# Optimization experiments

Measured on AMD Instinct MI355X. Metric: run time of the kernel, lower is better.

Reference implementation:

```python
import jax, jax.numpy as jnp
import numpy as np

B, C, O, H, W = 8, 64, 64, 128, 128


def conv3x3(x, w, b):
    # x: [B,Cin,H,W], w: [Cout,Cin,3,3], stride 1, padding 1
    y = jax.lax.conv_general_dilated(
        x, w, window_strides=(1, 1), padding=((1, 1), (1, 1)),
        dimension_numbers=("NCHW", "OIHW", "NCHW"))
    return y + b[None, :, None, None]


def setup_inputs() -> dict:
    key = jax.random.key(0)
    ks = jax.random.split(key, 6)
    fan = C * 9
    x = jax.random.normal(ks[0], (B, C, H, W), dtype=jnp.float32)
    w_main = jax.random.normal(ks[1], (O, C, 3, 3), dtype=jnp.float32) / np.sqrt(fan)
    # small offset weights keep sampled locations near the regular grid (realistic post-training regime)
    w_offset = jax.random.normal(ks[2], (18, C, 3, 3), dtype=jnp.float32) * 0.05 / np.sqrt(fan)
    b_offset = jnp.zeros((18,), dtype=jnp.float32)
    w_mask = jax.random.normal(ks[3], (9, C, 3, 3), dtype=jnp.float32) / np.sqrt(fan)
    b_mask = jnp.zeros((9,), dtype=jnp.float32)
    return {"x": x, "w_main": w_main, "w_offset": w_offset,
            "b_offset": b_offset, "w_mask": w_mask, "b_mask": b_mask}


def deform_conv2d(x, w_main, offset, mask):
    # torchvision.ops.deform_conv2d: kernel 3x3, stride 1, pad 1, dilation 1, no bias
    Bb, Cc, Hh, Ww = x.shape
    Oo = w_main.shape[0]
    off = offset.reshape(Bb, 9, 2, Hh, Ww)
    dy, dx = off[:, :, 0], off[:, :, 1]            # [B,9,H,W]; pairs ordered (y,x), k row-major
    k = jnp.arange(9)
    kh = (k // 3 - 1).astype(x.dtype)              # kernel row offset in {-1,0,1}
    kw = (k % 3 - 1).astype(x.dtype)
    iy = jnp.arange(Hh, dtype=x.dtype)
    ix = jnp.arange(Ww, dtype=x.dtype)
    # sampling positions p = p0 + p_k + delta_p
    py = dy + iy[None, None, :, None] + kh[None, :, None, None]
    px = dx + ix[None, None, None, :] + kw[None, :, None, None]

    y0 = jnp.floor(py)
    x0 = jnp.floor(px)
    ly = py - y0
    lx = px - x0
    y0i = y0.astype(jnp.int32)
    x0i = x0.astype(jnp.int32)
    y1i = y0i + 1
    x1i = x0i + 1

    bidx = jnp.arange(Bb)[:, None, None, None]

    def corner(yi, xi, wgt):
        # zero-padding semantics: out-of-bounds neighbors contribute 0
        valid = (yi >= 0) & (yi < Hh) & (xi >= 0) & (xi < Ww)
        v = x[bidx, :, jnp.clip(yi, 0, Hh - 1), jnp.clip(xi, 0, Ww - 1)]  # [B,9,H,W,C]
        return v * (wgt * valid)[..., None]

    samp = (corner(y0i, x0i, (1 - ly) * (1 - lx))
            + corner(y0i, x1i, (1 - ly) * lx)
            + corner(y1i, x0i, ly * (1 - lx))
            + corner(y1i, x1i, ly * lx))
    samp = samp * mask[..., None]                  # modulation mask (dcn v2)
    # contract sampled patches with weights: [B,9,H,W,C] x [O,C,9] -> [B,O,H,W]
    return jnp.einsum("bkhwc,ock->bohw", samp, w_main.reshape(Oo, Cc, 9))


def reference(x, w_main, w_offset, b_offset, w_mask, b_mask):
    offset = conv3x3(x, w_offset, b_offset)                 # [B,18,H,W]
    mask = jax.nn.sigmoid(conv3x3(x, w_mask, b_mask))       # [B,9,H,W]
    return deform_conv2d(x, w_main, offset, mask)
```

## Files before the change

kernel.cpp:

```cpp
#include <hip/hip_runtime.h>
#include <math.h>

#define BB 8
#define CC 64
#define OO 64
#define HH 128
#define WW 128
#define HW (HH*WW)
#define NPIX (BB*HW)

typedef __bf16 bf16x8 __attribute__((ext_vector_type(8)));
typedef float floatx4 __attribute__((ext_vector_type(4)));
typedef float f32x2 __attribute__((ext_vector_type(2)));
typedef unsigned short ushort_t;

#define XT_BYTES  16777216
#define OM_BYTES  14680064
#define WT_BYTES  73728

__device__ __forceinline__ unsigned short f2b(float f) {
    unsigned u = __float_as_uint(f);
    u += 0x7fffu + ((u >> 16) & 1u);
    return (unsigned short)(u >> 16);
}

__device__ __forceinline__ unsigned cvt_pk_bf16(float lo, float hi) {
    unsigned r;
    asm("v_cvt_pk_bf16_f32 %0, %1, %2" : "=v"(r) : "v"(lo), "v"(hi));
    return r;
}

__device__ __forceinline__ f32x2 pk_fma(f32x2 a, f32x2 b, f32x2 c) {
    f32x2 d;
    asm("v_pk_fma_f32 %0, %1, %2, %3" : "=v"(d) : "v"(a), "v"(b), "v"(c));
    return d;
}

__device__ __forceinline__ f32x2 pk_mul(f32x2 a, f32x2 b) {
    f32x2 d;
    asm("v_pk_mul_f32 %0, %1, %2" : "=v"(d) : "v"(a), "v"(b));
    return d;
}

__global__ __launch_bounds__(256) void prep_kernel(
    const float* __restrict__ x,
    const float* __restrict__ wm, const float* __restrict__ woff,
    const float* __restrict__ wmask,
    ushort_t* __restrict__ xt, ushort_t* __restrict__ wt,
    ushort_t* __restrict__ wb)
{
    __shared__ float tile[64][33];
    int bid = blockIdx.x;
    int t   = threadIdx.x;

    if (bid < 4096) {
        int bh = bid >> 2;
        int w0 = (bid & 3) * 32;
        int b  = bh >> 7;
        int h  = bh & 127;

        {
            int c  = t >> 2;
            int wq = t & 3;
            const float* src = x + (((size_t)(b*CC + c))*HH + h)*WW + (w0 + wq*8);
            float4 v0 = ((const float4*)src)[0];
            float4 v1 = ((const float4*)src)[1];
            int wbse = wq*8;
            tile[c][wbse+0] = v0.x; tile[c][wbse+1] = v0.y;
            tile[c][wbse+2] = v0.z; tile[c][wbse+3] = v0.w;
            tile[c][wbse+4] = v1.x; tile[c][wbse+5] = v1.y;
            tile[c][wbse+6] = v1.z; tile[c][wbse+7] = v1.w;
        }
        __syncthreads();
        {
            int w   = t & 31;
            int cg8 = t >> 5;
            unsigned uu[4];
            #pragma unroll
            for (int j = 0; j < 4; ++j)
                uu[j] = cvt_pk_bf16(tile[cg8*8 + 2*j][w], tile[cg8*8 + 2*j + 1][w]);
            *(uint4*)(xt + (((size_t)(b*HH + h))*WW + (w0 + w))*CC + cg8*8)
                = make_uint4(uu[0], uu[1], uu[2], uu[3]);
        }
    } else {
        int i = (bid - 4096) * 256 + t;
        if (i < 36864) {
            int o = i / 576, k = i % 576, tap = k >> 6, c = k & 63;
            wt[i] = f2b(wm[o*576 + c*9 + tap]);
        }
        int j = i - 36864;
        if (j >= 0 && j < 18432) {
            int o = j / 576, k = j % 576, tap = k >> 6, c = k & 63;
            float v = 0.f;
            if (o < 18)      v = woff[o*576 + c*9 + tap];
            else if (o < 27) v = wmask[(o-18)*576 + c*9 + tap];
            wb[j] = f2b(v);
        }
    }
}

__global__ __launch_bounds__(256) void conv27_kernel(
    const ushort_t* __restrict__ xt, const ushort_t* __restrict__ wb,
    const float* __restrict__ boff, const float* __restrict__ bmsk,
    float* __restrict__ om)
{
    __shared__ ushort_t win[18*18*72];
    int bid = blockIdx.x;
    int b  = bid >> 6;
    int th = (bid >> 3) & 7;
    int tw = bid & 7;
    int h0 = th * 16, w0 = tw * 16;
    int t = threadIdx.x;

    for (int idx = t; idx < 18*18*8; idx += 256) {
        int r   = idx / 144;
        int rem = idx - r*144;
        int col = rem >> 3;
        int ch  = (rem & 7) << 3;
        int y = h0 + r - 1, x = w0 + col - 1;
        uint4 val = make_uint4(0,0,0,0);
        if ((unsigned)y < (unsigned)HH && (unsigned)x < (unsigned)WW)
            val = *(const uint4*)(xt + ((((size_t)b*HH + y)*WW + x) << 6) + ch);
        *(uint4*)(win + (r*18 + col)*72 + ch) = val;
    }
    __syncthreads();

    int lane = t & 63, wv = t >> 6;
    int n = lane & 15, quad = lane >> 4;
    const ushort_t* wb0 = wb + n*576;
    const ushort_t* wb1 = wb + (16 + n)*576;

    floatx4 acc0[4], acc1[4];
    #pragma unroll
    for (int mt = 0; mt < 4; ++mt) {
        acc0[mt] = (floatx4){0.f,0.f,0.f,0.f};
        acc1[mt] = (floatx4){0.f,0.f,0.f,0.f};
    }

    #pragma unroll
    for (int s = 0; s < 18; ++s) {
        int tap  = s >> 1;
        int tr   = tap / 3, tc = tap % 3;
        int coff = (s & 1)*32 + quad*8;
        int kk = tap*64 + coff;
        bf16x8 b0 = *(const bf16x8*)(wb0 + kk);
        bf16x8 b1 = *(const bf16x8*)(wb1 + kk);
        #pragma unroll
        for (int mt = 0; mt < 4; ++mt) {
            int ty = wv*4 + mt;
            bf16x8 a = *(const bf16x8*)(win + ((ty + tr)*18 + (n + tc))*72 + coff);
            acc0[mt] = __builtin_amdgcn_mfma_f32_16x16x32_bf16(a, b0, acc0[mt], 0, 0, 0);
            acc1[mt] = __builtin_amdgcn_mfma_f32_16x16x32_bf16(a, b1, acc1[mt], 0, 0, 0);
        }
    }

    #pragma unroll
    for (int mt = 0; mt < 4; ++mt) {
        int ty = wv*4 + mt;
        #pragma unroll
        for (int r = 0; r < 4; ++r) {
            int tx = quad*4 + r;
            size_t p = ((size_t)(b*HH + h0 + ty))*WW + (w0 + tx);
            float* dst = om + p*28;
            dst[n] = acc0[mt][r] + boff[n];
            int o1 = 16 + n;
            if (o1 < 18) {
                dst[o1] = acc1[mt][r] + boff[o1];
            } else if (o1 < 27) {
                float z = acc1[mt][r] + bmsk[o1 - 18];
                dst[o1] = 1.f / (1.f + expf(-z));
            } else if (o1 == 27) {
                dst[27] = 0.f;
            }
        }
    }
}

#define SROW 200

__global__ __launch_bounds__(256, 3) void deform_kernel(
    const ushort_t* __restrict__ xt, const float* __restrict__ om,
    const ushort_t* __restrict__ wt, float* __restrict__ out)
{
    __shared__ ushort_t samp[64*SROW];

    int t = threadIdx.x;
    int lane = t & 63, wv = t >> 6;
    int bid = blockIdx.x;
    int b  = bid >> 8;
    int th = (bid >> 4) & 15;
    int tw = bid & 15;
    int h0 = th * 8, w0 = tw * 8;

    int pa = t >> 2, cg = t & 3;
    int ph = pa >> 3, pw = pa & 7;
    int h_a = h0 + ph, w_a = w0 + pw;
    const float* omp = om + (((size_t)(b*HH + h_a))*WW + w_a) * 28;
    const ushort_t* xbase = xt + ((size_t)b << 20);

    int n = lane & 15, quad = lane >> 4;
    floatx4 acc[4];
    #pragma unroll
    for (int i = 0; i < 4; ++i) acc[i] = (floatx4){0.f,0.f,0.f,0.f};
    const ushort_t* wrow = wt + (wv*16 + n)*576 + quad*8;

    uint4 q[24];
    float cwv[12];

    auto issue_phase = [&](int pp, const float* dy3, const float* dx3,
                           const float* m3) {
        #pragma unroll
        for (int kk = 0; kk < 3; ++kk) {
            float py = (float)(h_a + pp - 1) + dy3[kk];
            float px = (float)(w_a + kk - 1) + dx3[kk];
            float y0f = floorf(py), x0f = floorf(px);
            float ly = py - y0f, lx = px - x0f;
            int y0 = (int)y0f, x0 = (int)x0f, y1 = y0 + 1, x1 = x0 + 1;
            float vy0 = ((unsigned)y0 < (unsigned)HH) ? 1.f : 0.f;
            float vy1 = ((unsigned)y1 < (unsigned)HH) ? 1.f : 0.f;
            float vx0 = ((unsigned)x0 < (unsigned)WW) ? 1.f : 0.f;
            float vx1 = ((unsigned)x1 < (unsigned)WW) ? 1.f : 0.f;
            float m   = m3[kk];
            cwv[kk*4+0] = (1.f-ly)*(1.f-lx)*vy0*vx0*m;
            cwv[kk*4+1] = (1.f-ly)*lx      *vy0*vx1*m;
            cwv[kk*4+2] = ly*(1.f-lx)      *vy1*vx0*m;
            cwv[kk*4+3] = ly*lx            *vy1*vx1*m;
            int ys[4] = { y0, y0, y1, y1 };
            int xs[4] = { x0, x1, x0, x1 };
            #pragma unroll
            for (int cn = 0; cn < 4; ++cn) {
                int yc = min(max(ys[cn], 0), HH-1);
                int xc = min(max(xs[cn], 0), WW-1);
                const uint4* cp = (const uint4*)(xbase + (((yc << 7) + xc) << 6) + cg*16);
                q[kk*8+2*cn]   = cp[0];
                q[kk*8+2*cn+1] = cp[1];
            }
        }
    };

    float dyv[3], dxv[3], mv[3];
    #pragma unroll
    for (int j = 0; j < 3; ++j) {
        dyv[j] = omp[2*j]; dxv[j] = omp[2*j+1]; mv[j] = omp[18+j];
    }
    issue_phase(0, dyv, dxv, mv);

    #pragma unroll
    for (int p = 0; p < 3; ++p) {
        bf16x8 wf[6];
        #pragma unroll
        for (int s = 0; s < 6; ++s)
            wf[s] = *(const bf16x8*)(wrow + (p*6 + s)*32);

        float dyn_[3], dxn_[3], mn_[3];
        if (p < 2) {
            #pragma unroll
            for (int j = 0; j < 3; ++j) {
                int k2 = 3*(p+1) + j;
                dyn_[j] = omp[2*k2]; dxn_[j] = omp[2*k2+1]; mn_[j] = omp[18+k2];
            }
        }

        if (p) __syncthreads();

        #pragma unroll
        for (int kk = 0; kk < 3; ++kk) {
            f32x2 v2[8];
            {
                f32x2 w2; w2.x = cwv[kk*4+0]; w2.y = cwv[kk*4+0];
                unsigned u0[8] = { q[kk*8+0].x, q[kk*8+0].y, q[kk*8+0].z, q[kk*8+0].w,
                                   q[kk*8+1].x, q[kk*8+1].y, q[kk*8+1].z, q[kk*8+1].w };
                #pragma unroll
                for (int j = 0; j < 8; ++j) {
                    f32x2 f;
                    f.x = __uint_as_float(u0[j] << 16);
                    f.y = __uint_as_float(u0[j] & 0xffff0000u);
                    v2[j] = pk_mul(f, w2);
                }
            }
            #pragma unroll
            for (int cn = 1; cn < 4; ++cn) {
                f32x2 w2; w2.x = cwv[kk*4+cn]; w2.y = cwv[kk*4+cn];
                unsigned u0[8] = { q[kk*8+2*cn].x,   q[kk*8+2*cn].y,
                                   q[kk*8+2*cn].z,   q[kk*8+2*cn].w,
                                   q[kk*8+2*cn+1].x, q[kk*8+2*cn+1].y,
                                   q[kk*8+2*cn+1].z, q[kk*8+2*cn+1].w };
                #pragma unroll
                for (int j = 0; j < 8; ++j) {
                    f32x2 f;
                    f.x = __uint_as_float(u0[j] << 16);
                    f.y = __uint_as_float(u0[j] & 0xffff0000u);
                    v2[j] = pk_fma(f, w2, v2[j]);
                }
            }
            unsigned uu[8];
            #pragma unroll
            for (int j = 0; j < 8; ++j)
                uu[j] = cvt_pk_bf16(v2[j].x, v2[j].y);
            uint4* dst = (uint4*)(samp + pa*SROW + kk*64 + cg*16);
            dst[0] = make_uint4(uu[0], uu[1], uu[2], uu[3]);
            dst[1] = make_uint4(uu[4], uu[5], uu[6], uu[7]);
        }

        if (p < 2) issue_phase(p+1, dyn_, dxn_, mn_);

        __syncthreads();

        __builtin_amdgcn_s_setprio(1);
        #pragma unroll
        for (int kk = 0; kk < 3; ++kk) {
            #pragma unroll
            for (int half = 0; half < 2; ++half) {
                bf16x8 bfrag = wf[kk*2 + half];
                #pragma unroll
                for (int mt = 0; mt < 4; ++mt) {
                    bf16x8 afrag = *(const bf16x8*)(samp + (mt*16 + n)*SROW
                                                    + kk*64 + half*32 + quad*8);
                    acc[mt] = __builtin_amdgcn_mfma_f32_16x16x32_bf16(
                                  afrag, bfrag, acc[mt], 0, 0, 0);
                }
            }
        }
        __builtin_amdgcn_s_setprio(0);
    }

    float* op = out + ((size_t)b*OO + (wv*16 + n))*HW;
    #pragma unroll
    for (int mt = 0; mt < 4; ++mt) {
        int row = h0 + mt*2 + (quad >> 1);
        int col = w0 + (quad & 1)*4;
        float4 st = make_float4(acc[mt][0], acc[mt][1], acc[mt][2], acc[mt][3]);
        *(float4*)(op + row*WW + col) = st;
    }
}

extern "C" void kernel_launch(void* const* d_in, const int* in_sizes, int n_in,
                              void* d_out, int out_size, void* d_ws, size_t ws_size,
                              hipStream_t stream)
{
    const float* x      = (const float*)d_in[0];
    const float* w_main = (const float*)d_in[1];
    const float* w_off  = (const float*)d_in[2];
    const float* b_off  = (const float*)d_in[3];
    const float* w_msk  = (const float*)d_in[4];
    const float* b_msk  = (const float*)d_in[5];
    float* out = (float*)d_out;

    unsigned char* ws = (unsigned char*)d_ws;
    ushort_t* xt = (ushort_t*)ws;
    float*    om = (float*)(ws + XT_BYTES);
    ushort_t* wt = (ushort_t*)(ws + XT_BYTES + OM_BYTES);
    ushort_t* wb = (ushort_t*)(ws + XT_BYTES + OM_BYTES + WT_BYTES);

    prep_kernel<<<4096 + 216, 256, 0, stream>>>(x, w_main, w_off, w_msk, xt, wt, wb);

    conv27_kernel<<<NPIX/256, 256, 0, stream>>>(xt, wb, b_off, b_msk, om);

    deform_kernel<<<NPIX/64, 256, 0, stream>>>(xt, om, wt, out);
}
```

Before: 175.8 us.

## Pipeline bilinear gathers per tap with double-buffered registers instead of per-row phases

```diff
diff --git a/kernel.cpp b/kernel.cpp
--- a/kernel.cpp
+++ b/kernel.cpp
@@ -176,6 +176,74 @@
     }
 }
 
+__device__ __forceinline__ void issue_tap(
+    uint4* q, float* cw,
+    const ushort_t* xbase, int cg, int h_a, int w_a,
+    int kr, int kc, float dy, float dx, float m)
+{
+    float py = (float)(h_a + kr - 1) + dy;
+    float px = (float)(w_a + kc - 1) + dx;
+    float y0f = floorf(py), x0f = floorf(px);
+    float ly = py - y0f, lx = px - x0f;
+    int y0 = (int)y0f, x0 = (int)x0f, y1 = y0 + 1, x1 = x0 + 1;
+    float vy0 = ((unsigned)y0 < (unsigned)HH) ? 1.f : 0.f;
+    float vy1 = ((unsigned)y1 < (unsigned)HH) ? 1.f : 0.f;
+    float vx0 = ((unsigned)x0 < (unsigned)WW) ? 1.f : 0.f;
+    float vx1 = ((unsigned)x1 < (unsigned)WW) ? 1.f : 0.f;
+    cw[0] = (1.f-ly)*(1.f-lx)*vy0*vx0*m;
+    cw[1] = (1.f-ly)*lx      *vy0*vx1*m;
+    cw[2] = ly*(1.f-lx)      *vy1*vx0*m;
+    cw[3] = ly*lx            *vy1*vx1*m;
+    int ys[4] = { y0, y0, y1, y1 };
+    int xs[4] = { x0, x1, x0, x1 };
+    #pragma unroll
+    for (int cn = 0; cn < 4; ++cn) {
+        int yc = min(max(ys[cn], 0), HH-1);
+        int xc = min(max(xs[cn], 0), WW-1);
+        const uint4* cp = (const uint4*)(xbase + (((yc << 7) + xc) << 6) + cg*16);
+        q[2*cn]   = cp[0];
+        q[2*cn+1] = cp[1];
+    }
+}
+
+__device__ __forceinline__ void pack_tap(
+    const uint4* q, const float* cw, ushort_t* dst)
+{
+    f32x2 v2[8];
+    {
+        f32x2 w2; w2.x = cw[0]; w2.y = cw[0];
+        unsigned u0[8] = { q[0].x, q[0].y, q[0].z, q[0].w,
+                           q[1].x, q[1].y, q[1].z, q[1].w };
+        #pragma unroll
+        for (int j = 0; j < 8; ++j) {
+            f32x2 f;
+            f.x = __uint_as_float(u0[j] << 16);
+            f.y = __uint_as_float(u0[j] & 0xffff0000u);
+            v2[j] = pk_mul(f, w2);
+        }
+    }
+    #pragma unroll
+    for (int cn = 1; cn < 4; ++cn) {
+        f32x2 w2; w2.x = cw[cn]; w2.y = cw[cn];
+        unsigned u0[8] = { q[2*cn].x,   q[2*cn].y,   q[2*cn].z,   q[2*cn].w,
+                           q[2*cn+1].x, q[2*cn+1].y, q[2*cn+1].z, q[2*cn+1].w };
+        #pragma unroll
+        for (int j = 0; j < 8; ++j) {
+            f32x2 f;
+            f.x = __uint_as_float(u0[j] << 16);
+            f.y = __uint_as_float(u0[j] & 0xffff0000u);
+            v2[j] = pk_fma(f, w2, v2[j]);
+        }
+    }
+    unsigned uu[8];
+    #pragma unroll
+    for (int j = 0; j < 8; ++j)
+        uu[j] = cvt_pk_bf16(v2[j].x, v2[j].y);
+    uint4* d = (uint4*)dst;
+    d[0] = make_uint4(uu[0], uu[1], uu[2], uu[3]);
+    d[1] = make_uint4(uu[4], uu[5], uu[6], uu[7]);
+}
+
 #define SROW 200
 
 __global__ __launch_bounds__(256, 3) void deform_kernel(
@@ -204,46 +272,15 @@
     for (int i = 0; i < 4; ++i) acc[i] = (floatx4){0.f,0.f,0.f,0.f};
     const ushort_t* wrow = wt + (wv*16 + n)*576 + quad*8;
 
-    uint4 q[24];
-    float cwv[12];
-
-    auto issue_phase = [&](int pp, const float* dy3, const float* dx3,
-                           const float* m3) {
-        #pragma unroll
-        for (int kk = 0; kk < 3; ++kk) {
-            float py = (float)(h_a + pp - 1) + dy3[kk];
-            float px = (float)(w_a + kk - 1) + dx3[kk];
-            float y0f = floorf(py), x0f = floorf(px);
-            float ly = py - y0f, lx = px - x0f;
-            int y0 = (int)y0f, x0 = (int)x0f, y1 = y0 + 1, x1 = x0 + 1;
-            float vy0 = ((unsigned)y0 < (unsigned)HH) ? 1.f : 0.f;
-            float vy1 = ((unsigned)y1 < (unsigned)HH) ? 1.f : 0.f;
-            float vx0 = ((unsigned)x0 < (unsigned)WW) ? 1.f : 0.f;
-            float vx1 = ((unsigned)x1 < (unsigned)WW) ? 1.f : 0.f;
-            float m   = m3[kk];
-            cwv[kk*4+0] = (1.f-ly)*(1.f-lx)*vy0*vx0*m;
-            cwv[kk*4+1] = (1.f-ly)*lx      *vy0*vx1*m;
-            cwv[kk*4+2] = ly*(1.f-lx)      *vy1*vx0*m;
-            cwv[kk*4+3] = ly*lx            *vy1*vx1*m;
-            int ys[4] = { y0, y0, y1, y1 };
-            int xs[4] = { x0, x1, x0, x1 };
-            #pragma unroll
-            for (int cn = 0; cn < 4; ++cn) {
-                int yc = min(max(ys[cn], 0), HH-1);
-                int xc = min(max(xs[cn], 0), WW-1);
-                const uint4* cp = (const uint4*)(xbase + (((yc << 7) + xc) << 6) + cg*16);
-                q[kk*8+2*cn]   = cp[0];
-                q[kk*8+2*cn+1] = cp[1];
-            }
-        }
-    };
+    uint4 q[2][8];
+    float cw[2][4];
 
     float dyv[3], dxv[3], mv[3];
     #pragma unroll
     for (int j = 0; j < 3; ++j) {
         dyv[j] = omp[2*j]; dxv[j] = omp[2*j+1]; mv[j] = omp[18+j];
     }
-    issue_phase(0, dyv, dxv, mv);
+    issue_tap(q[0], cw[0], xbase, cg, h_a, w_a, 0, 0, dyv[0], dxv[0], mv[0]);
 
     #pragma unroll
     for (int p = 0; p < 3; ++p) {
@@ -261,48 +298,19 @@
             }
         }
 
-        if (p) __syncthreads();
-
         #pragma unroll
         for (int kk = 0; kk < 3; ++kk) {
-            f32x2 v2[8];
-            {
-                f32x2 w2; w2.x = cwv[kk*4+0]; w2.y = cwv[kk*4+0];
-                unsigned u0[8] = { q[kk*8+0].x, q[kk*8+0].y, q[kk*8+0].z, q[kk*8+0].w,
-                                   q[kk*8+1].x, q[kk*8+1].y, q[kk*8+1].z, q[kk*8+1].w };
-                #pragma unroll
-                for (int j = 0; j < 8; ++j) {
-                    f32x2 f;
-                    f.x = __uint_as_float(u0[j] << 16);
-                    f.y = __uint_as_float(u0[j] & 0xffff0000u);
-                    v2[j] = pk_mul(f, w2);
-                }
-            }
-            #pragma unroll
-            for (int cn = 1; cn < 4; ++cn) {
-                f32x2 w2; w2.x = cwv[kk*4+cn]; w2.y = cwv[kk*4+cn];
-                unsigned u0[8] = { q[kk*8+2*cn].x,   q[kk*8+2*cn].y,
-                                   q[kk*8+2*cn].z,   q[kk*8+2*cn].w,
-                                   q[kk*8+2*cn+1].x, q[kk*8+2*cn+1].y,
-                                   q[kk*8+2*cn+1].z, q[kk*8+2*cn+1].w };
-                #pragma unroll
-                for (int j = 0; j < 8; ++j) {
-                    f32x2 f;
-                    f.x = __uint_as_float(u0[j] << 16);
-                    f.y = __uint_as_float(u0[j] & 0xffff0000u);
-                    v2[j] = pk_fma(f, w2, v2[j]);
-                }
-            }
-            unsigned uu[8];
-            #pragma unroll
-            for (int j = 0; j < 8; ++j)
-                uu[j] = cvt_pk_bf16(v2[j].x, v2[j].y);
-            uint4* dst = (uint4*)(samp + pa*SROW + kk*64 + cg*16);
-            dst[0] = make_uint4(uu[0], uu[1], uu[2], uu[3]);
-            dst[1] = make_uint4(uu[4], uu[5], uu[6], uu[7]);
-        }
-
-        if (p < 2) issue_phase(p+1, dyn_, dxn_, mn_);
+            int g = 3*p + kk;
+            if (g < 8) {
+                if (kk < 2)
+                    issue_tap(q[(g+1)&1], cw[(g+1)&1], xbase, cg, h_a, w_a,
+                              p, kk+1, dyv[kk+1], dxv[kk+1], mv[kk+1]);
+                else
+                    issue_tap(q[(g+1)&1], cw[(g+1)&1], xbase, cg, h_a, w_a,
+                              p+1, 0, dyn_[0], dxn_[0], mn_[0]);
+            }
+            pack_tap(q[g&1], cw[g&1], samp + pa*SROW + kk*64 + cg*16);
+        }
 
         __syncthreads();
 
@@ -322,6 +330,14 @@
             }
         }
         __builtin_amdgcn_s_setprio(0);
+
+        if (p < 2) {
+            __syncthreads();
+            #pragma unroll
+            for (int j = 0; j < 3; ++j) {
+                dyv[j] = dyn_[j]; dxv[j] = dxn_[j]; mv[j] = mn_[j];
+            }
+        }
     }
 
     float* op = out + ((size_t)b*OO + (wv*16 + n))*HW;
```

After: 158.0 us. 10.1% less time.
